# Optimization experiments

Measured on AMD Instinct MI355X. Metric: run time of the kernel, lower is better.

The kernel has to match this reference:

```python
import jax, jax.numpy as jnp
import numpy as np

B, S, F, D, U, DS = 128, 64, 32, 128, 128, 128  # batch, seq, features, feat_dim, units, static_dim
DIN = S * F * D + DS  # grn_concat input dim
EPS = 1e-3  # keras LayerNormalization default epsilon


def _ln(x, gamma, beta):
    m = jnp.mean(x, axis=-1, keepdims=True)
    v = jnp.mean(jnp.square(x - m), axis=-1, keepdims=True)
    return (x - m) * jax.lax.rsqrt(v + EPS) * gamma + beta


def setup_inputs() -> dict:
    key = jax.random.key(0)
    ks = iter(jax.random.split(key, 32))
    p = lambda *shape: jax.random.normal(next(ks), shape, dtype=jnp.float32) * 0.02
    inp = {
        "inputs": jax.random.normal(next(ks), (B, S, F * D), dtype=jnp.float32),
        "static_input": jax.random.normal(next(ks), (B, DS), dtype=jnp.float32),
        # grn_concat (input dim DIN != U -> project path active)
        "cWe": p(DIN, U), "cbe": jnp.zeros((U,), jnp.float32),
        "cWl": p(U, U), "cbl": jnp.zeros((U,), jnp.float32),
        "cWgl": p(U, U), "cbgl": jnp.zeros((U,), jnp.float32),
        "cWgs": p(U, U), "cbgs": jnp.zeros((U,), jnp.float32),
        "cgamma": jnp.ones((U,), jnp.float32), "cbeta": jnp.zeros((U,), jnp.float32),
        "cWp": p(DIN, U), "cbp": jnp.zeros((U,), jnp.float32),
        # softmax Dense: units -> num_features
        "Ws": p(U, F), "bs": jnp.zeros((F,), jnp.float32),
        # per-feature GRNs, stacked over feature axis (feat_dim == units -> no project)
        "fWe": p(F, D, U), "fbe": jnp.zeros((F, U), jnp.float32),
        "fWl": p(F, U, U), "fbl": jnp.zeros((F, U), jnp.float32),
        "fWgl": p(F, U, U), "fbgl": jnp.zeros((F, U), jnp.float32),
        "fWgs": p(F, U, U), "fbgs": jnp.zeros((F, U), jnp.float32),
        "fgamma": jnp.ones((F, U), jnp.float32), "fbeta": jnp.zeros((F, U), jnp.float32),
    }
    return inp


def reference(inputs, static_input, cWe, cbe, cWl, cbl, cWgl, cbgl, cWgs, cbgs,
              cgamma, cbeta, cWp, cbp, Ws, bs, fWe, fbe, fWl, fbl, fWgl, fbgl,
              fWgs, fbgs, fgamma, fbeta):
    b = inputs.shape[0]
    # --- selection weights: flatten + concat static, grn_concat, softmax dense ---
    v = jnp.concatenate([inputs.reshape(b, -1), static_input], axis=-1)  # [B, DIN]
    h = jax.nn.elu(v @ cWe + cbe)
    h = h @ cWl + cbl
    res = v @ cWp + cbp  # project (DIN != U)
    g = (h @ cWgl + cbgl) * jax.nn.sigmoid(h @ cWgs + cbgs)  # GLU
    y = _ln(res + g, cgamma, cbeta)  # [B, U]
    w = jax.nn.softmax(y @ Ws + bs, axis=-1)  # [B, F]
    # --- per-feature GRNs, batched over feature axis ---
    x = inputs.reshape(b, S, F, D)  # tf.split along axis 2
    h = jax.nn.elu(jnp.einsum('bsfd,fdu->bsfu', x, fWe) + fbe)
    h = jnp.einsum('bsfu,fuv->bsfv', h, fWl) + fbl
    g = (jnp.einsum('bsfu,fuv->bsfv', h, fWgl) + fbgl) * \
        jax.nn.sigmoid(jnp.einsum('bsfu,fuv->bsfv', h, fWgs) + fbgs)
    xg = _ln(x + g, fgamma, fbeta)  # [B, S, F, U]
    # --- softmax-weighted combine (v repeated over seq, matmul transpose_a) ---
    out = jnp.einsum('bf,bsfu->bsu', w, xg)  # [B, S, U]
    return out
```

## Files before the change

### kernel.cpp

```cpp
#include <hip/hip_runtime.h>


typedef unsigned short u16;
typedef __attribute__((ext_vector_type(4))) u16 u16x4;
typedef __attribute__((ext_vector_type(8))) u16 u16x8;
typedef __attribute__((ext_vector_type(8))) __bf16 bf16x8;
typedef __attribute__((ext_vector_type(4))) float f32x4;

__device__ __forceinline__ u16 f2bf(float f) {
  unsigned int x = __float_as_uint(f);
  return (u16)((x + 0x7fffu + ((x >> 16) & 1u)) >> 16);
}
__device__ __forceinline__ float eluf(float x) { return x > 0.f ? x : __expf(x) - 1.f; }
__device__ __forceinline__ float sigmoidf_(float x) { return 1.f / (1.f + __expf(-x)); }

#define MFMA_BF16(a, b, c) __builtin_amdgcn_mfma_f32_16x16x32_bf16((a), (b), (c), 0, 0, 0)

__global__ __launch_bounds__(128) void k0_prep(
    const float* __restrict__ fWe, const float* __restrict__ fWl,
    const float* __restrict__ fWgl, const float* __restrict__ fWgs,
    u16* __restrict__ wT)
{
  const int b = blockIdx.x, f = b >> 2, mat = b & 3;
  const float* srcs[4] = {fWe, fWl, fWgl, fWgs};
  const float* src = srcs[mat] + (size_t)f * 16384;
  u16* dst = wT + (size_t)b * 16384;
  const int n = threadIdx.x;
  for (int k8 = 0; k8 < 16; ++k8) {
    u16x8 p;
#pragma unroll
    for (int j = 0; j < 8; ++j) p[j] = f2bf(src[(k8 * 8 + j) * 128 + n]);
    *(u16x8*)&dst[n * 128 + k8 * 8] = p;
  }
}

__global__ __launch_bounds__(1024) void k1_bigmm(
    const float* __restrict__ inp, const float* __restrict__ cWe,
    const float* __restrict__ cWp, float* __restrict__ outE, float* __restrict__ outP)
{
  __shared__ __align__(16) u16 xA[2][128][72];
  __shared__ __align__(16) u16 wE[2][128][72];
  __shared__ __align__(16) u16 wP[2][128][72];
  const int t = threadIdx.x;
  const int lane = t & 63, wv = t >> 6, quad = lane >> 4, l16 = lane & 15;
  const int mat = wv >> 3, wvm = wv & 7;
  const int wt = t & 511, wmi = t >> 9;
  const int k4g = wt >> 5, nb4 = wt & 31;
  const float* Wm = wmi ? cWp : cWe;

  f32x4 acc[8];
#pragma unroll
  for (int n = 0; n < 8; ++n)
#pragma unroll
    for (int r = 0; r < 4; ++r) acc[n][r] = 0.f;

  const size_t kbase = (size_t)blockIdx.x * 1024;

  float4 avr[2], wvr[4];
  auto load_regs = [&](int it) {
    const size_t kk = kbase + (size_t)it * 64;
#pragma unroll
    for (int i = 0; i < 2; ++i) {
      const int idx = t + i * 1024;
      const int row = idx >> 4, fo = idx & 15;
      avr[i] = *(const float4*)(inp + (size_t)row * 262144 + kk + fo * 4);
    }
#pragma unroll
    for (int j = 0; j < 4; ++j)
      wvr[j] = *(const float4*)(Wm + (kk + (size_t)(k4g * 4 + j)) * 128 + nb4 * 4);
  };
  auto store_lds = [&](int buf) {
#pragma unroll
    for (int i = 0; i < 2; ++i) {
      const int idx = t + i * 1024;
      const int row = idx >> 4, fo = idx & 15;
      u16x4 p; p[0] = f2bf(avr[i].x); p[1] = f2bf(avr[i].y);
      p[2] = f2bf(avr[i].z); p[3] = f2bf(avr[i].w);
      *(u16x4*)&xA[buf][row][fo * 4] = p;
    }
    u16 (*Wl)[72] = wmi ? wP[buf] : wE[buf];
#pragma unroll
    for (int c = 0; c < 4; ++c) {
      u16x4 col;
      col[0] = f2bf(((const float*)&wvr[0])[c]);
      col[1] = f2bf(((const float*)&wvr[1])[c]);
      col[2] = f2bf(((const float*)&wvr[2])[c]);
      col[3] = f2bf(((const float*)&wvr[3])[c]);
      *(u16x4*)&Wl[nb4 * 4 + c][k4g * 4] = col;
    }
  };

  load_regs(0);
  store_lds(0);
  for (int it = 0; it < 16; ++it) {
    const int buf = it & 1;
    __syncthreads();
    if (it < 15) load_regs(it + 1);
    u16 (*Wb)[72] = mat ? wP[buf] : wE[buf];
#pragma unroll
    for (int ks = 0; ks < 2; ++ks) {
      const int ko = ks * 32 + quad * 8;
      const bf16x8 a = *(const bf16x8*)&xA[buf][16 * wvm + l16][ko];
#pragma unroll
      for (int nt = 0; nt < 8; ++nt) {
        const bf16x8 b = *(const bf16x8*)&Wb[nt * 16 + l16][ko];
        acc[nt] = MFMA_BF16(a, b, acc[nt]);
      }
    }
    if (it < 15) store_lds(buf ^ 1);
  }
  float* outp = mat ? outP : outE;
#pragma unroll
  for (int nt = 0; nt < 8; ++nt) {
    const int col = nt * 16 + l16;
#pragma unroll
    for (int r = 0; r < 4; ++r) {
      const int row = 16 * wvm + quad * 4 + r;
      atomicAdd(&outp[row * 128 + col], acc[nt][r]);
    }
  }
}

__global__ __launch_bounds__(512) void k1b_small(
    const float* __restrict__ stat,
    const float* __restrict__ cWe, const float* __restrict__ cbe,
    const float* __restrict__ cWl, const float* __restrict__ cbl,
    const float* __restrict__ cWgl, const float* __restrict__ cbgl,
    const float* __restrict__ cWgs, const float* __restrict__ cbgs,
    const float* __restrict__ cgam, const float* __restrict__ cbet,
    const float* __restrict__ cWp, const float* __restrict__ cbp,
    const float* __restrict__ Ws, const float* __restrict__ bs,
    const float* __restrict__ preE, const float* __restrict__ preP,
    float* __restrict__ wout)
{
  const int b = blockIdx.x, t = threadIdx.x;
  const int u = t & 127, dc = t >> 7;
  __shared__ float shS[128], shA[128], shB[128], par[8][132], red[4];
  if (t < 128) shS[t] = stat[b * 128 + t];
  __syncthreads();

  const float* we = cWe + (size_t)262144 * 128;
  const float* wp = cWp + (size_t)262144 * 128;
  float hp = 0.f, rp = 0.f;
  for (int d = dc * 32; d < dc * 32 + 32; ++d) {
    const float sv = shS[d];
    hp += sv * we[d * 128 + u];
    rp += sv * wp[d * 128 + u];
  }
  par[dc][u] = hp; par[4 + dc][u] = rp;
  __syncthreads();

  float rs = 0.f;
  if (t < 128) {
    const float he = preE[b * 128 + t] + cbe[t] + par[0][t] + par[1][t] + par[2][t] + par[3][t];
    rs = preP[b * 128 + t] + cbp[t] + par[4][t] + par[5][t] + par[6][t] + par[7][t];
    shA[t] = eluf(he);
  }
  __syncthreads();

  float p = 0.f;
  for (int d = dc * 32; d < dc * 32 + 32; ++d) p += shA[d] * cWl[d * 128 + u];
  par[dc][u] = p;
  __syncthreads();
  if (t < 128) shB[t] = cbl[t] + par[0][t] + par[1][t] + par[2][t] + par[3][t];
  __syncthreads();

  float gp = 0.f, sp = 0.f;
  for (int d = dc * 32; d < dc * 32 + 32; ++d) {
    const float hv = shB[d];
    gp += hv * cWgl[d * 128 + u];
    sp += hv * cWgs[d * 128 + u];
  }
  par[dc][u] = gp; par[4 + dc][u] = sp;
  __syncthreads();

  float z = 0.f;
  if (t < 128) {
    const float gl = cbgl[t] + par[0][t] + par[1][t] + par[2][t] + par[3][t];
    const float gs = cbgs[t] + par[4][t] + par[5][t] + par[6][t] + par[7][t];
    z = rs + gl * sigmoidf_(gs);
  }
  float s = z, q = z * z;
#pragma unroll
  for (int off = 32; off >= 1; off >>= 1) { s += __shfl_xor(s, off); q += __shfl_xor(q, off); }
  if ((t & 63) == 0 && t < 128) { red[(t >> 6) * 2] = s; red[(t >> 6) * 2 + 1] = q; }
  __syncthreads();
  if (t < 128) {
    const float S = red[0] + red[2], Q = red[1] + red[3];
    const float mean = S * (1.f / 128.f);
    const float var = Q * (1.f / 128.f) - mean * mean;
    const float rstd = rsqrtf(var + 1e-3f);
    shA[t] = (z - mean) * rstd * cgam[t] + cbet[t];
  }
  __syncthreads();
  if (t < 32) {
    float sj = bs[t];
    for (int uu = 0; uu < 128; ++uu) sj += shA[uu] * Ws[uu * 32 + t];
    float m = sj;
#pragma unroll
    for (int off = 16; off >= 1; off >>= 1) m = fmaxf(m, __shfl_xor(m, off));
    const float e = __expf(sj - m);
    float se = e;
#pragma unroll
    for (int off = 16; off >= 1; off >>= 1) se += __shfl_xor(se, off);
    wout[b * 32 + t] = e / se;
  }
}

__device__ __forceinline__ void stage_wt(const u16* __restrict__ src, int kh,
                                         u16 WT[][72], int t)
{
#pragma unroll
  for (int i = 0; i < 4; ++i) {
    const int u = t + i * 256;
    const int n = u >> 3, k8 = u & 7;
    *(u16x8*)&WT[n][k8 * 8] = *(const u16x8*)(src + n * 128 + kh + k8 * 8);
  }
}

__device__ __forceinline__ void mm_half(const u16 A[][136], const u16 WT[][72],
                                        int wv, int quad, int l16, int kh, f32x4 acc[8])
{
#pragma unroll
  for (int ks = 0; ks < 2; ++ks) {
    const int kol = ks * 32 + quad * 8;
    const bf16x8 a = *(const bf16x8*)&A[16 * wv + l16][kh + kol];
#pragma unroll
    for (int nt = 0; nt < 8; ++nt) {
      const bf16x8 b = *(const bf16x8*)&WT[nt * 16 + l16][kol];
      acc[nt] = MFMA_BF16(a, b, acc[nt]);
    }
  }
}

__global__ __launch_bounds__(256) void k2_grn(
    const float* __restrict__ inp, const u16* __restrict__ wT,
    const float* __restrict__ fbe, const float* __restrict__ fbl,
    const float* __restrict__ fbgl, const float* __restrict__ fbgs,
    const float* __restrict__ fgam, const float* __restrict__ fbet,
    const float* __restrict__ wsel, float* __restrict__ out)
{
  __shared__ __align__(16) u16 xA[64][136];
  __shared__ __align__(16) u16 hA[64][136];
  __shared__ __align__(16) u16 WT[128][72];
  const int t = threadIdx.x;
  const int lane = t & 63, wv = t >> 6, quad = lane >> 4, l16 = lane & 15;
  const int bb = blockIdx.x & 127, fg = blockIdx.x >> 7;

  f32x4 acc[8], glr[8], racc[8];
#pragma unroll
  for (int n = 0; n < 8; ++n)
#pragma unroll
    for (int r = 0; r < 4; ++r) racc[n][r] = 0.f;

#define ZERO_ACC() do { _Pragma("unroll") \
  for (int n_ = 0; n_ < 8; ++n_) { acc[n_][0]=0.f; acc[n_][1]=0.f; acc[n_][2]=0.f; acc[n_][3]=0.f; } } while (0)

  for (int fi = 0; fi < 8; ++fi) {
    const int f = fg * 8 + fi;
    const float wb = wsel[bb * 32 + f];
    const u16* wf = wT + (size_t)f * 65536;

    __syncthreads();
#pragma unroll
    for (int i = 0; i < 8; ++i) {
      const int u = t + i * 256;
      const int row = u >> 5, fo = u & 31;
      const float4 v = *(const float4*)(inp + (size_t)(bb * 64 + row) * 4096 + f * 128 + fo * 4);
      u16x4 p; p[0] = f2bf(v.x); p[1] = f2bf(v.y); p[2] = f2bf(v.z); p[3] = f2bf(v.w);
      *(u16x4*)&xA[row][fo * 4] = p;
    }

    stage_wt(wf, 0, WT, t);
    __syncthreads();
    ZERO_ACC();
    mm_half(xA, WT, wv, quad, l16, 0, acc);
    __syncthreads();
    stage_wt(wf, 64, WT, t);
    __syncthreads();
    mm_half(xA, WT, wv, quad, l16, 64, acc);
#pragma unroll
    for (int nt = 0; nt < 8; ++nt) {
      const int col = nt * 16 + l16;
      const float bv = fbe[f * 128 + col];
#pragma unroll
      for (int r = 0; r < 4; ++r)
        hA[16 * wv + quad * 4 + r][col] = f2bf(eluf(acc[nt][r] + bv));
    }
    __syncthreads();

    stage_wt(wf + 16384, 0, WT, t);
    __syncthreads();
    ZERO_ACC();
    mm_half(hA, WT, wv, quad, l16, 0, acc);
    __syncthreads();
    stage_wt(wf + 16384, 64, WT, t);
    __syncthreads();
    mm_half(hA, WT, wv, quad, l16, 64, acc);
#pragma unroll
    for (int nt = 0; nt < 8; ++nt) {
      const int col = nt * 16 + l16;
      const float bv = fbl[f * 128 + col];
#pragma unroll
      for (int r = 0; r < 4; ++r)
        hA[16 * wv + quad * 4 + r][col] = f2bf(acc[nt][r] + bv);
    }
    __syncthreads();

    stage_wt(wf + 2 * 16384, 0, WT, t);
    __syncthreads();
    ZERO_ACC();
    mm_half(hA, WT, wv, quad, l16, 0, acc);
    __syncthreads();
    stage_wt(wf + 2 * 16384, 64, WT, t);
    __syncthreads();
    mm_half(hA, WT, wv, quad, l16, 64, acc);
#pragma unroll
    for (int nt = 0; nt < 8; ++nt) {
      const int col = nt * 16 + l16;
      const float bv = fbgl[f * 128 + col];
#pragma unroll
      for (int r = 0; r < 4; ++r) glr[nt][r] = acc[nt][r] + bv;
    }
    __syncthreads();

    stage_wt(wf + 3 * 16384, 0, WT, t);
    __syncthreads();
    ZERO_ACC();
    mm_half(hA, WT, wv, quad, l16, 0, acc);
    __syncthreads();
    stage_wt(wf + 3 * 16384, 64, WT, t);
    __syncthreads();
    mm_half(hA, WT, wv, quad, l16, 64, acc);

#pragma unroll
    for (int nt = 0; nt < 8; ++nt) {
      const int col = nt * 16 + l16;
      const float bv = fbgs[f * 128 + col];
#pragma unroll
      for (int r = 0; r < 4; ++r) {
        const float g = glr[nt][r] * sigmoidf_(acc[nt][r] + bv);
        const float x = __uint_as_float(((unsigned int)xA[16 * wv + quad * 4 + r][col]) << 16);
        acc[nt][r] = x + g;
      }
    }
    float sm[4], sq[4];
#pragma unroll
    for (int r = 0; r < 4; ++r) {
      float s = 0.f, q = 0.f;
#pragma unroll
      for (int nt = 0; nt < 8; ++nt) { const float zz = acc[nt][r]; s += zz; q += zz * zz; }
      sm[r] = s; sq[r] = q;
    }
#pragma unroll
    for (int off = 1; off <= 8; off <<= 1)
#pragma unroll
      for (int r = 0; r < 4; ++r) { sm[r] += __shfl_xor(sm[r], off); sq[r] += __shfl_xor(sq[r], off); }
#pragma unroll
    for (int r = 0; r < 4; ++r) {
      const float mean = sm[r] * (1.f / 128.f);
      const float var = sq[r] * (1.f / 128.f) - mean * mean;
      const float rstd = rsqrtf(var + 1e-3f);
      sm[r] = mean; sq[r] = rstd;
    }
#pragma unroll
    for (int nt = 0; nt < 8; ++nt) {
      const int col = nt * 16 + l16;
      const float gam = fgam[f * 128 + col];
      const float bet = fbet[f * 128 + col];
#pragma unroll
      for (int r = 0; r < 4; ++r) {
        const float xg = (acc[nt][r] - sm[r]) * sq[r] * gam + bet;
        racc[nt][r] += wb * xg;
      }
    }
  }

#pragma unroll
  for (int nt = 0; nt < 8; ++nt) {
    const int col = nt * 16 + l16;
#pragma unroll
    for (int r = 0; r < 4; ++r) {
      const int grow = bb * 64 + 16 * wv + quad * 4 + r;
      atomicAdd(&out[(size_t)grow * 128 + col], racc[nt][r]);
    }
  }
#undef ZERO_ACC
}

extern "C" void kernel_launch(void* const* d_in, const int* in_sizes, int n_in,
                              void* d_out, int out_size, void* d_ws, size_t ws_size,
                              hipStream_t stream)
{
  const float* inp    = (const float*)d_in[0];
  const float* stat   = (const float*)d_in[1];
  const float* cWe    = (const float*)d_in[2];
  const float* cbe    = (const float*)d_in[3];
  const float* cWl    = (const float*)d_in[4];
  const float* cbl    = (const float*)d_in[5];
  const float* cWgl   = (const float*)d_in[6];
  const float* cbgl   = (const float*)d_in[7];
  const float* cWgs   = (const float*)d_in[8];
  const float* cbgs   = (const float*)d_in[9];
  const float* cgamma = (const float*)d_in[10];
  const float* cbeta  = (const float*)d_in[11];
  const float* cWp    = (const float*)d_in[12];
  const float* cbp    = (const float*)d_in[13];
  const float* Ws     = (const float*)d_in[14];
  const float* bs     = (const float*)d_in[15];
  const float* fWe    = (const float*)d_in[16];
  const float* fbe    = (const float*)d_in[17];
  const float* fWl    = (const float*)d_in[18];
  const float* fbl    = (const float*)d_in[19];
  const float* fWgl   = (const float*)d_in[20];
  const float* fbgl   = (const float*)d_in[21];
  const float* fWgs   = (const float*)d_in[22];
  const float* fbgs   = (const float*)d_in[23];
  const float* fgam   = (const float*)d_in[24];
  const float* fbet   = (const float*)d_in[25];

  float* ws_he  = (float*)d_ws;
  float* ws_res = ws_he + 16384;
  float* ws_w   = ws_res + 16384;
  u16*   ws_wT  = (u16*)(ws_w + 4096);

  hipMemsetAsync(d_ws, 0, 32768 * sizeof(float), stream);
  hipMemsetAsync(d_out, 0, (size_t)out_size * sizeof(float), stream);
  k0_prep<<<128, 128, 0, stream>>>(fWe, fWl, fWgl, fWgs, ws_wT);
  k1_bigmm<<<256, 1024, 0, stream>>>(inp, cWe, cWp, ws_he, ws_res);
  k1b_small<<<128, 512, 0, stream>>>(stat, cWe, cbe, cWl, cbl, cWgl, cbgl, cWgs, cbgs,
                                     cgamma, cbeta, cWp, cbp, Ws, bs, ws_he, ws_res, ws_w);
  k2_grn<<<512, 256, 0, stream>>>(inp, ws_wT, fbe, fbl, fbgl, fbgs,
                                  fgam, fbet, ws_w, (float*)d_out);
}
```

Before: 575.0 us.

## Split-K big GEMM into per-block partial slabs plus separate reduction kernel

Restructures the large flattened-input projection GEMM: blocks shrink to 512 threads with a K-step of 32 and two M-subtiles per wave. The K split is chosen from the available workspace (up to 512 blocks). When the workspace allows, each block writes its partial result to its own slab and a new reduce kernel sums the slabs, replacing the fp32 atomics on the output. The weight-transpose prep kernel also switches to vectorized float4 loads over an 8x8 register tile. This trades atomic contention and low occupancy for extra workspace traffic and one more kernel launch.

```diff
diff --git a/kernel.cpp b/kernel.cpp
--- a/kernel.cpp
+++ b/kernel.cpp
@@ -16,7 +16,7 @@
 
 #define MFMA_BF16(a, b, c) __builtin_amdgcn_mfma_f32_16x16x32_bf16((a), (b), (c), 0, 0, 0)
 
-__global__ __launch_bounds__(128) void k0_prep(
+__global__ __launch_bounds__(256) void k0_prep(
     const float* __restrict__ fWe, const float* __restrict__ fWl,
     const float* __restrict__ fWgl, const float* __restrict__ fWgs,
     u16* __restrict__ wT)
@@ -25,100 +25,138 @@
   const float* srcs[4] = {fWe, fWl, fWgl, fWgs};
   const float* src = srcs[mat] + (size_t)f * 16384;
   u16* dst = wT + (size_t)b * 16384;
-  const int n = threadIdx.x;
-  for (int k8 = 0; k8 < 16; ++k8) {
+  const int ti = threadIdx.x >> 4, tj = threadIdx.x & 15;
+  float r[8][8];
+#pragma unroll
+  for (int j = 0; j < 8; ++j) {
+    const float4 v0 = *(const float4*)(src + (size_t)(ti * 8 + j) * 128 + tj * 8);
+    const float4 v1 = *(const float4*)(src + (size_t)(ti * 8 + j) * 128 + tj * 8 + 4);
+    r[j][0] = v0.x; r[j][1] = v0.y; r[j][2] = v0.z; r[j][3] = v0.w;
+    r[j][4] = v1.x; r[j][5] = v1.y; r[j][6] = v1.z; r[j][7] = v1.w;
+  }
+#pragma unroll
+  for (int c = 0; c < 8; ++c) {
     u16x8 p;
 #pragma unroll
-    for (int j = 0; j < 8; ++j) p[j] = f2bf(src[(k8 * 8 + j) * 128 + n]);
-    *(u16x8*)&dst[n * 128 + k8 * 8] = p;
-  }
-}
-
-__global__ __launch_bounds__(1024) void k1_bigmm(
+    for (int j = 0; j < 8; ++j) p[j] = f2bf(r[j][c]);
+    *(u16x8*)(dst + (size_t)(tj * 8 + c) * 128 + ti * 8) = p;
+  }
+}
+
+__global__ __launch_bounds__(512, 4) void k1_bigmm(
     const float* __restrict__ inp, const float* __restrict__ cWe,
-    const float* __restrict__ cWp, float* __restrict__ outE, float* __restrict__ outP)
-{
-  __shared__ __align__(16) u16 xA[2][128][72];
-  __shared__ __align__(16) u16 wE[2][128][72];
-  __shared__ __align__(16) u16 wP[2][128][72];
+    const float* __restrict__ cWp, float* __restrict__ part,
+    float* __restrict__ heE, float* __restrict__ heP,
+    int kiters, int slabMode)
+{
+  __shared__ __align__(16) u16 xA[2][128][40];
+  __shared__ __align__(16) u16 wE[2][128][40];
+  __shared__ __align__(16) u16 wP[2][128][40];
   const int t = threadIdx.x;
   const int lane = t & 63, wv = t >> 6, quad = lane >> 4, l16 = lane & 15;
-  const int mat = wv >> 3, wvm = wv & 7;
-  const int wt = t & 511, wmi = t >> 9;
-  const int k4g = wt >> 5, nb4 = wt & 31;
+  const int mat = wv >> 2, mq = wv & 3;
+  const int arow = t >> 3, afo = t & 7;
+  const int wmi = t >> 8;
+  const int tt = t & 255, km = tt >> 5, nb = tt & 31;
   const float* Wm = wmi ? cWp : cWe;
 
-  f32x4 acc[8];
-#pragma unroll
-  for (int n = 0; n < 8; ++n)
-#pragma unroll
-    for (int r = 0; r < 4; ++r) acc[n][r] = 0.f;
-
-  const size_t kbase = (size_t)blockIdx.x * 1024;
+  f32x4 acc[2][8];
+#pragma unroll
+  for (int m = 0; m < 2; ++m)
+#pragma unroll
+    for (int n = 0; n < 8; ++n) { acc[m][n][0]=0.f; acc[m][n][1]=0.f; acc[m][n][2]=0.f; acc[m][n][3]=0.f; }
+
+  const size_t kbase = (size_t)blockIdx.x * kiters * 32;
 
   float4 avr[2], wvr[4];
   auto load_regs = [&](int it) {
-    const size_t kk = kbase + (size_t)it * 64;
-#pragma unroll
-    for (int i = 0; i < 2; ++i) {
-      const int idx = t + i * 1024;
-      const int row = idx >> 4, fo = idx & 15;
-      avr[i] = *(const float4*)(inp + (size_t)row * 262144 + kk + fo * 4);
-    }
+    const size_t kk = kbase + (size_t)it * 32;
+    avr[0] = *(const float4*)(inp + (size_t)arow * 262144 + kk + afo * 4);
+    avr[1] = *(const float4*)(inp + (size_t)(arow + 64) * 262144 + kk + afo * 4);
 #pragma unroll
     for (int j = 0; j < 4; ++j)
-      wvr[j] = *(const float4*)(Wm + (kk + (size_t)(k4g * 4 + j)) * 128 + nb4 * 4);
+      wvr[j] = *(const float4*)(Wm + (kk + (size_t)(km * 4 + j)) * 128 + nb * 4);
   };
   auto store_lds = [&](int buf) {
-#pragma unroll
-    for (int i = 0; i < 2; ++i) {
-      const int idx = t + i * 1024;
-      const int row = idx >> 4, fo = idx & 15;
-      u16x4 p; p[0] = f2bf(avr[i].x); p[1] = f2bf(avr[i].y);
-      p[2] = f2bf(avr[i].z); p[3] = f2bf(avr[i].w);
-      *(u16x4*)&xA[buf][row][fo * 4] = p;
-    }
-    u16 (*Wl)[72] = wmi ? wP[buf] : wE[buf];
+    u16x4 p0, p1;
+    p0[0] = f2bf(avr[0].x); p0[1] = f2bf(avr[0].y); p0[2] = f2bf(avr[0].z); p0[3] = f2bf(avr[0].w);
+    p1[0] = f2bf(avr[1].x); p1[1] = f2bf(avr[1].y); p1[2] = f2bf(avr[1].z); p1[3] = f2bf(avr[1].w);
+    *(u16x4*)&xA[buf][arow][afo * 4] = p0;
+    *(u16x4*)&xA[buf][arow + 64][afo * 4] = p1;
+    u16 (*Wl)[40] = wmi ? wP[buf] : wE[buf];
 #pragma unroll
     for (int c = 0; c < 4; ++c) {
-      u16x4 col;
-      col[0] = f2bf(((const float*)&wvr[0])[c]);
-      col[1] = f2bf(((const float*)&wvr[1])[c]);
-      col[2] = f2bf(((const float*)&wvr[2])[c]);
-      col[3] = f2bf(((const float*)&wvr[3])[c]);
-      *(u16x4*)&Wl[nb4 * 4 + c][k4g * 4] = col;
+      u16x4 q;
+      q[0] = f2bf(((const float*)&wvr[0])[c]);
+      q[1] = f2bf(((const float*)&wvr[1])[c]);
+      q[2] = f2bf(((const float*)&wvr[2])[c]);
+      q[3] = f2bf(((const float*)&wvr[3])[c]);
+      *(u16x4*)&Wl[nb * 4 + c][km * 4] = q;
     }
   };
 
   load_regs(0);
   store_lds(0);
-  for (int it = 0; it < 16; ++it) {
+  for (int it = 0; it < kiters; ++it) {
     const int buf = it & 1;
     __syncthreads();
-    if (it < 15) load_regs(it + 1);
-    u16 (*Wb)[72] = mat ? wP[buf] : wE[buf];
-#pragma unroll
-    for (int ks = 0; ks < 2; ++ks) {
-      const int ko = ks * 32 + quad * 8;
-      const bf16x8 a = *(const bf16x8*)&xA[buf][16 * wvm + l16][ko];
-#pragma unroll
-      for (int nt = 0; nt < 8; ++nt) {
-        const bf16x8 b = *(const bf16x8*)&Wb[nt * 16 + l16][ko];
-        acc[nt] = MFMA_BF16(a, b, acc[nt]);
-      }
-    }
-    if (it < 15) store_lds(buf ^ 1);
-  }
-  float* outp = mat ? outP : outE;
-#pragma unroll
-  for (int nt = 0; nt < 8; ++nt) {
-    const int col = nt * 16 + l16;
-#pragma unroll
-    for (int r = 0; r < 4; ++r) {
-      const int row = 16 * wvm + quad * 4 + r;
-      atomicAdd(&outp[row * 128 + col], acc[nt][r]);
-    }
-  }
+    if (it + 1 < kiters) load_regs(it + 1);
+    u16 (*Wb)[40] = mat ? wP[buf] : wE[buf];
+    const int ko = quad * 8;
+    const bf16x8 a0 = *(const bf16x8*)&xA[buf][32 * mq + l16][ko];
+    const bf16x8 a1 = *(const bf16x8*)&xA[buf][32 * mq + 16 + l16][ko];
+#pragma unroll
+    for (int nt = 0; nt < 8; ++nt) {
+      const bf16x8 bfr = *(const bf16x8*)&Wb[nt * 16 + l16][ko];
+      acc[0][nt] = MFMA_BF16(a0, bfr, acc[0][nt]);
+      acc[1][nt] = MFMA_BF16(a1, bfr, acc[1][nt]);
+    }
+    if (it + 1 < kiters) store_lds(buf ^ 1);
+  }
+
+  if (slabMode) {
+    float* dst = part + (size_t)blockIdx.x * 32768 + (size_t)mat * 16384;
+#pragma unroll
+    for (int m = 0; m < 2; ++m)
+#pragma unroll
+      for (int nt = 0; nt < 8; ++nt)
+#pragma unroll
+        for (int r = 0; r < 4; ++r) {
+          const int row = 32 * mq + m * 16 + quad * 4 + r;
+          dst[row * 128 + nt * 16 + l16] = acc[m][nt][r];
+        }
+  } else {
+    float* dst = mat ? heP : heE;
+#pragma unroll
+    for (int m = 0; m < 2; ++m)
+#pragma unroll
+      for (int nt = 0; nt < 8; ++nt)
+#pragma unroll
+        for (int r = 0; r < 4; ++r) {
+          const int row = 32 * mq + m * 16 + quad * 4 + r;
+          atomicAdd(&dst[row * 128 + nt * 16 + l16], acc[m][nt][r]);
+        }
+  }
+}
+
+__global__ __launch_bounds__(256) void k1_reduce(
+    const float* __restrict__ part, float* __restrict__ he, int nkb)
+{
+  const int gid = blockIdx.x * 256 + threadIdx.x;
+  const int e4 = gid & 8191;
+  const int ks = gid >> 13;
+  const int slice = nkb >> 4;
+  f32x4 s0 = {0.f,0.f,0.f,0.f}, s1 = {0.f,0.f,0.f,0.f};
+  const float* p = part + (size_t)(ks * slice) * 32768 + (size_t)e4 * 4;
+  for (int i = 0; i < slice; i += 2) {
+    const f32x4 v0 = *(const f32x4*)(p + (size_t)i * 32768);
+    const f32x4 v1 = *(const f32x4*)(p + (size_t)(i + 1) * 32768);
+    s0 += v0; s1 += v1;
+  }
+  s0 += s1;
+  float* o = he + e4 * 4;
+  atomicAdd(&o[0], s0[0]); atomicAdd(&o[1], s0[1]);
+  atomicAdd(&o[2], s0[2]); atomicAdd(&o[3], s0[3]);
 }
 
 __global__ __launch_bounds__(512) void k1b_small(
@@ -408,26 +446,40 @@
   const float* cbp    = (const float*)d_in[13];
   const float* Ws     = (const float*)d_in[14];
   const float* bs     = (const float*)d_in[15];
-  const float* fWe    = (const float*)d_in[16];
   const float* fbe    = (const float*)d_in[17];
-  const float* fWl    = (const float*)d_in[18];
   const float* fbl    = (const float*)d_in[19];
-  const float* fWgl   = (const float*)d_in[20];
   const float* fbgl   = (const float*)d_in[21];
-  const float* fWgs   = (const float*)d_in[22];
   const float* fbgs   = (const float*)d_in[23];
   const float* fgam   = (const float*)d_in[24];
   const float* fbet   = (const float*)d_in[25];
+  const float* fWe    = (const float*)d_in[16];
+  const float* fWl    = (const float*)d_in[18];
+  const float* fWgl   = (const float*)d_in[20];
+  const float* fWgs   = (const float*)d_in[22];
 
   float* ws_he  = (float*)d_ws;
   float* ws_res = ws_he + 16384;
-  float* ws_w   = ws_res + 16384;
-  u16*   ws_wT  = (u16*)(ws_w + 4096);
-
-  hipMemsetAsync(d_ws, 0, 32768 * sizeof(float), stream);
+  float* ws_w   = ws_he + 32768;
+  u16*   ws_wT  = (u16*)(ws_he + 36864);
+  float* ws_sl  = ws_he + 1085440;
+
+  int nkb = 0;
+  const size_t base_bytes = (size_t)1085440 * 4;
+  for (int cand = 512; cand >= 64; cand >>= 1) {
+    if (ws_size >= base_bytes + (size_t)cand * 32768 * 4) { nkb = cand; break; }
+  }
+
   hipMemsetAsync(d_out, 0, (size_t)out_size * sizeof(float), stream);
-  k0_prep<<<128, 128, 0, stream>>>(fWe, fWl, fWgl, fWgs, ws_wT);
-  k1_bigmm<<<256, 1024, 0, stream>>>(inp, cWe, cWp, ws_he, ws_res);
+  hipMemsetAsync(ws_he, 0, 32768 * sizeof(float), stream);
+  k0_prep<<<128, 256, 0, stream>>>(fWe, fWl, fWgl, fWgs, ws_wT);
+
+  if (nkb > 0) {
+    const int kiters = 8192 / nkb;
+    k1_bigmm<<<nkb, 512, 0, stream>>>(inp, cWe, cWp, ws_sl, ws_he, ws_res, kiters, 1);
+    k1_reduce<<<512, 256, 0, stream>>>(ws_sl, ws_he, nkb);
+  } else {
+    k1_bigmm<<<256, 512, 0, stream>>>(inp, cWe, cWp, ws_sl, ws_he, ws_res, 32, 0);
+  }
   k1b_small<<<128, 512, 0, stream>>>(stat, cWe, cbe, cWl, cbl, cWgl, cbgl, cWgs, cbgs,
                                      cgamma, cbeta, cWp, cbp, Ws, bs, ws_he, ws_res, ws_w);
   k2_grn<<<512, 256, 0, stream>>>(inp, ws_wT, fbe, fbl, fbgl, fbgs,
```

Result: slower. 592.0 us (+2.9%).
